# Kernel tuning notes

Hardware: AMD Instinct MI355X
Metric: run time of the kernel (lower is better)

## Reference

```python
import jax, jax.numpy as jnp
from jax import lax
import numpy as np

KSIZE = 3      # match-patch size
STRIDE = 1
RATE = 2       # down/up-sampling rate
FUSE_K = 3
SCALE = 10.0   # softmax scale
DN = ('NHWC', 'HWIO', 'NHWC')


def extract_patches(x, k, s):
    """tf.image.extract_patches(..., padding='SAME'); returns [B, L, k, k, C]."""
    B, H, W, C = x.shape
    oh, ow = -(-H // s), -(-W // s)
    ph = max((oh - 1) * s + k - H, 0)
    pw = max((ow - 1) * s + k - W, 0)
    xp = jnp.pad(x, ((0, 0), (ph // 2, ph - ph // 2), (pw // 2, pw - pw // 2), (0, 0)))
    cols = [xp[:, i:i + oh * s:s, j:j + ow * s:s, :] for i in range(k) for j in range(k)]
    p = jnp.stack(cols, axis=3)                 # [B, oh, ow, k*k, C]
    return p.reshape(B, oh * ow, k, k, C)


def setup_inputs() -> dict:
    key = jax.random.key(0)
    k1, k2, k3 = jax.random.split(key, 3)
    B, H, W, C = 4, 96, 96, 64
    f = jax.random.normal(k1, (B, H, W, C), jnp.float32)
    b = jax.random.normal(k2, (B, H, W, C), jnp.float32)
    mask = jnp.zeros((B, H, W, 1), jnp.float32)          # 0 = no hole -> all patches valid
    fuse_weight = jax.random.normal(k3, (FUSE_K, FUSE_K, 1, 1), jnp.float32) * 0.3
    return {"f": f, "b": b, "mask": mask, "fuse_weight": fuse_weight}


def reference(f, b, mask, fuse_weight):
    B, H, W, C = f.shape
    kernel = 2 * RATE
    # deconv kernels from full-res background: [B, 4, 4, C, L]
    raw_w = extract_patches(b, kernel, RATE * STRIDE).transpose(0, 2, 3, 4, 1)
    fd = f[:, 1::2, 1::2, :]
    bd = b[:, 1::2, 1::2, :]
    md = mask[:, 1::2, 1::2, :]
    h, w_ = fd.shape[1], fd.shape[2]
    L = h * w_
    # matching kernels from downscaled background: [B, 3, 3, C, L]
    wk = extract_patches(bd, KSIZE, STRIDE).transpose(0, 2, 3, 4, 1)
    # mask patches -> per-patch validity mm: [B, L]
    mp = extract_patches(md, KSIZE, STRIDE)
    mm = (jnp.mean(mp, axis=(2, 3, 4)) == 0.0).astype(f.dtype)

    def per_sample(xi, wi, rwi, mmi):
        # xi: [h, w, C]; wi: [3,3,C,L]; rwi: [4,4,C,L]; mmi: [L]
        norm = jnp.maximum(jnp.sqrt(jnp.sum(wi * wi, axis=(0, 1, 2))), 1e-4)
        yi = lax.conv_general_dilated(xi[None], wi / norm, (1, 1), 'SAME',
                                      dimension_numbers=DN)[0]        # [h, w, L]
        # fuse: 3x3 conv over flattened [HW, HW] score map, twice (transposed view)
        y = yi.reshape(1, L, L, 1)
        y = lax.conv_general_dilated(y, fuse_weight, (1, 1), 'SAME', dimension_numbers=DN)
        y = y.reshape(h, w_, h, w_).transpose(1, 0, 3, 2).reshape(1, L, L, 1)
        y = lax.conv_general_dilated(y, fuse_weight, (1, 1), 'SAME', dimension_numbers=DN)
        y = y.reshape(w_, h, w_, h).transpose(1, 0, 3, 2).reshape(h, w_, L)
        # mask-gated scaled softmax over background patches
        y = y * mmi
        y = jax.nn.softmax(y * SCALE, axis=-1) * mmi
        # deconv-style combine with raw 4x4 patches, stride=rate
        out = lax.conv_transpose(y[None], rwi, (RATE, RATE), 'SAME',
                                 dimension_numbers=DN, transpose_kernel=True)[0] / 4.0
        return out                                                    # [H, W, C]

    return jax.vmap(per_sample)(fd, wk, raw_w, mm)
```

## Files before the change

### kernel.cpp

```cpp
#include <hip/hip_runtime.h>
#include <hip/hip_bf16.h>

#define KL  2304
#define KC  64
#define KHS 48
#define KHH 96
#define OFFY (KHS*(KL + 1))

typedef __attribute__((ext_vector_type(8))) short bf16x8;
typedef __attribute__((ext_vector_type(4))) short bf16x4;
typedef __attribute__((ext_vector_type(8))) _Float16 f16x8;
typedef __attribute__((ext_vector_type(4))) _Float16 f16x4;
typedef __attribute__((ext_vector_type(4))) float f32x4;

static __device__ inline unsigned short f2bf(float x) {
    __hip_bfloat16 h = __float2bfloat16(x);
    return *reinterpret_cast<unsigned short*>(&h);
}
static __device__ inline float bf2f(unsigned short u) {
    unsigned v = ((unsigned)u) << 16;
    return __uint_as_float(v);
}
static __device__ inline unsigned short f2h(float x) {
    _Float16 h = (_Float16)x;
    return *reinterpret_cast<unsigned short*>(&h);
}
static __device__ inline float h2f(unsigned short u) {
    _Float16 h = *reinterpret_cast<_Float16*>(&u);
    return (float)h;
}

__global__ __launch_bounds__(64) void k_prep2(const float* __restrict__ f,
    const float* __restrict__ bsrc, const float* __restrict__ mask,
    float* __restrict__ nbuf, float* __restrict__ mdd,
    unsigned short* __restrict__ Ahat, unsigned short* __restrict__ Bhat)
{
    int blk = blockIdx.x;
    int p = blk % KL, bi = blk / KL;
    int y = p / KHS, x = p % KHS;
    int fy = 2*y + 1;
    int c = threadIdx.x;
    unsigned short* Ap = Ahat + ((size_t)bi*KL + p)*192;
    unsigned short* Bp = Bhat + ((size_t)bi*KL + p)*192;
    float bc = 0.f;
    #pragma unroll
    for (int dxi = 0; dxi < 3; dxi++) {
        int xx = x + dxi - 1;
        float av = 0.f, bv = 0.f;
        if ((unsigned)xx < KHS) {
            int fxx = 2*xx + 1;
            size_t src = (((size_t)bi*KHH + fy)*KHH + fxx)*KC + c;
            av = f[src]; bv = bsrc[src];
        }
        if (dxi == 1) bc = bv;
        Ap[dxi*64 + c] = f2h(av);
        Bp[dxi*64 + c] = f2h(bv);
    }
    float s = bc*bc;
    #pragma unroll
    for (int off = 32; off > 0; off >>= 1) s += __shfl_down(s, off);
    if (c == 0) {
        nbuf[bi*KL + p] = s;
        mdd[bi*KL + p]  = mask[((size_t)bi*KHH + fy)*KHH + (2*x + 1)];
    }
}

__global__ __launch_bounds__(256) void k_normmask(const float* __restrict__ nbuf,
    const float* __restrict__ mdd, float* __restrict__ rnrm, float* __restrict__ mm)
{
    int i = blockIdx.x*256 + threadIdx.x;
    int q = i % KL, bi = i / KL;
    int v = q / KHS, u = q % KHS;
    float sn = 0.f, sm = 0.f;
    for (int dy = -1; dy <= 1; dy++) {
        int vv = v + dy; if ((unsigned)vv >= KHS) continue;
        for (int dx = -1; dx <= 1; dx++) {
            int uu = u + dx; if ((unsigned)uu >= KHS) continue;
            sn += nbuf[bi*KL + vv*KHS + uu];
            sm += mdd[bi*KL + vv*KHS + uu];
        }
    }
    rnrm[i] = 1.0f / fmaxf(sqrtf(sn), 1e-4f);
    mm[i]   = (sm == 0.0f) ? 1.0f : 0.0f;
}

template<int KITERS, int OUTMODE, bool INFP16>
__global__ __launch_bounds__(256) void k_mfma_bt(const unsigned short* __restrict__ A,
    const unsigned short* __restrict__ B, void* __restrict__ Cv,
    int Ncols, size_t sA, size_t sB, size_t sC, int KDIM, int nsplit, size_t psize)
{
    int flat = blockIdx.x + gridDim.x*(blockIdx.y + gridDim.y*blockIdx.z);
    int nxy = gridDim.x*gridDim.y;
    int per = (nxy*gridDim.z) >> 3;
    int g = (flat & 7)*per + (flat >> 3);
    int z = g / nxy; int r = g - z*nxy;
    int by = r / gridDim.x; int bx = r - by*gridDim.x;

    int ks = z % nsplit, bi = z / nsplit;
    int kbase = ks * KITERS * 32;
    int n0 = bx*128, m0 = by*128;
    const unsigned short* Ab = A + (size_t)bi*sA;
    const unsigned short* Bb = B + (size_t)bi*sB;
    __shared__ unsigned short As[128*32];
    __shared__ unsigned short Bs[128*32];
    int t = threadIdx.x;
    int lane = t & 63, w = t >> 6;
    int l15 = lane & 15, quad = lane >> 4;
    int swf = (l15 >> 2) & 3;
    int wm = (w >> 1)*64, wn = (w & 1)*64;
    int srow = lane >> 2;
    int ch = lane & 3;
    f32x4 acc[4][4];
    #pragma unroll
    for (int i = 0; i < 4; i++)
        #pragma unroll
        for (int j = 0; j < 4; j++) acc[i][j] = (f32x4){0.f,0.f,0.f,0.f};

    for (int kk = 0; kk < KITERS; kk++) {
        int k0 = kbase + kk*32;
        #pragma unroll
        for (int i = 0; i < 2; i++) {
            int rbase = w*32 + i*16;
            int r2 = rbase + srow;
            int cs = (ch ^ ((r2 >> 2) & 3))*8;
            const unsigned short* ga = &Ab[(size_t)(m0 + r2)*KDIM + k0 + cs];
            __builtin_amdgcn_global_load_lds(
                (const __attribute__((address_space(1))) void*)ga,
                (__attribute__((address_space(3))) void*)&As[rbase*32], 16, 0, 0);
            const unsigned short* gb = &Bb[(size_t)(n0 + r2)*KDIM + k0 + cs];
            __builtin_amdgcn_global_load_lds(
                (const __attribute__((address_space(1))) void*)gb,
                (__attribute__((address_space(3))) void*)&Bs[rbase*32], 16, 0, 0);
        }
        __syncthreads();
        if (INFP16) {
            f16x8 af[4], bfr[4];
            #pragma unroll
            for (int mi = 0; mi < 4; mi++)
                af[mi] = *(const f16x8*)&As[(wm + mi*16 + l15)*32 + ((quad ^ swf)*8)];
            #pragma unroll
            for (int ni = 0; ni < 4; ni++)
                bfr[ni] = *(const f16x8*)&Bs[(wn + ni*16 + l15)*32 + ((quad ^ swf)*8)];
            #pragma unroll
            for (int mi = 0; mi < 4; mi++)
                #pragma unroll
                for (int ni = 0; ni < 4; ni++)
                    acc[mi][ni] = __builtin_amdgcn_mfma_f32_16x16x32_f16(
                        af[mi], bfr[ni], acc[mi][ni], 0, 0, 0);
        } else {
            bf16x8 af[4], bfr[4];
            #pragma unroll
            for (int mi = 0; mi < 4; mi++)
                af[mi] = *(const bf16x8*)&As[(wm + mi*16 + l15)*32 + ((quad ^ swf)*8)];
            #pragma unroll
            for (int ni = 0; ni < 4; ni++)
                bfr[ni] = *(const bf16x8*)&Bs[(wn + ni*16 + l15)*32 + ((quad ^ swf)*8)];
            #pragma unroll
            for (int mi = 0; mi < 4; mi++)
                #pragma unroll
                for (int ni = 0; ni < 4; ni++)
                    acc[mi][ni] = __builtin_amdgcn_mfma_f32_16x16x32_bf16(
                        af[mi], bfr[ni], acc[mi][ni], 0, 0, 0);
        }
        __syncthreads();
    }
    if (OUTMODE == 1 || OUTMODE == 2) {
        unsigned short* Cb = (unsigned short*)Cv + (size_t)ks*psize + (size_t)bi*sC;
        #pragma unroll
        for (int mi = 0; mi < 4; mi++)
            #pragma unroll
            for (int ni = 0; ni < 4; ni++) {
                int col = n0 + wn + ni*16 + l15;
                #pragma unroll
                for (int r2 = 0; r2 < 4; r2++) {
                    int row = m0 + wm + mi*16 + quad*4 + r2;
                    Cb[(size_t)row*Ncols + col] = (OUTMODE == 1)
                        ? f2bf(acc[mi][ni][r2]) : f2h(acc[mi][ni][r2]);
                }
            }
    } else {
        float* Cb = (float*)Cv + (size_t)ks*psize + (size_t)bi*sC;
        #pragma unroll
        for (int mi = 0; mi < 4; mi++)
            #pragma unroll
            for (int ni = 0; ni < 4; ni++) {
                int col = n0 + wn + ni*16 + l15;
                #pragma unroll
                for (int r2 = 0; r2 < 4; r2++) {
                    int row = m0 + wm + mi*16 + quad*4 + r2;
                    Cb[(size_t)row*Ncols + col] = acc[mi][ni][r2];
                }
            }
    }
}

#define KP_NT 18
#define STGA4(tt, j) do {                                                      \
    __builtin_amdgcn_global_load_lds(                                          \
        (const __attribute__((address_space(1))) void*)(gA + (size_t)(j)*128*2304 + (size_t)(tt)*32), \
        (__attribute__((address_space(3))) void*)&Atile[(tt)&3][((j)*128 + (w<<4))*32], 16, 0, 0); \
} while (0)
#define STGB4(tt, j) do {                                                      \
    __builtin_amdgcn_global_load_lds(                                          \
        (const __attribute__((address_space(1))) void*)(gB + (size_t)(j)*128*2304 + (size_t)(tt)*32), \
        (__attribute__((address_space(3))) void*)&Btile[(tt)&3][((j)*128 + (w<<4))*32], 16, 0, 0); \
} while (0)

#define MFMA_B(a, b, c) __builtin_amdgcn_mfma_f32_16x16x32_bf16(a, b, c, 0, 0, 0)

#define KT_BODY(kt, BVU, BVF) do {                                             \
    const unsigned short* At = &Atile[(kt) & 3][0];                            \
                                                          \
    __builtin_amdgcn_s_barrier();                                              \
    _Pragma("unroll")                                                          \
    for (int i = 0; i < 4; i++)                                                \
        af1[i] = *(const bf16x8*)&At[aOff + 2048 + i*512];                     \
    if ((kt) + 3 < KP_NT) { STGA4((kt)+3, 0); STGA4((kt)+3, 1); }              \
    __builtin_amdgcn_s_setprio(1);                                             \
    _Pragma("unroll")                                                          \
    for (int mi = 0; mi < 4; mi++)                                             \
        _Pragma("unroll")                                                      \
        for (int ni = 0; ni < 4; ni++)                                         \
            acc[mi][ni] = MFMA_B(af0[mi], BVU[ni], acc[mi][ni]);               \
    __builtin_amdgcn_s_setprio(0);                                             \
                                                          \
    __builtin_amdgcn_s_barrier();                                              \
    if ((kt) < KP_NT-1) {                                                      \
        if ((kt) <= KP_NT-4)      asm volatile("s_waitcnt vmcnt(6)" ::: "memory"); \
        else if ((kt) == KP_NT-3) asm volatile("s_waitcnt vmcnt(4)" ::: "memory"); \
        else                      asm volatile("s_waitcnt vmcnt(0)" ::: "memory"); \
        __builtin_amdgcn_sched_barrier(0);                                     \
        const unsigned short* An = &Atile[((kt)+1) & 3][0];                    \
        const unsigned short* Bn = &Btile[((kt)+1) & 3][0];                    \
        _Pragma("unroll")                                                      \
        for (int i = 0; i < 4; i++)                                            \
            af0[i] = *(const bf16x8*)&An[aOff + i*512];                        \
        _Pragma("unroll")                                                      \
        for (int ni = 0; ni < 4; ni++)                                         \
            BVF[ni] = *(const bf16x8*)&Bn[bOff + ni*512];                      \
    }                                                                          \
    if ((kt) + 3 < KP_NT) { STGB4((kt)+3, 0); STGB4((kt)+3, 1); }              \
    __builtin_amdgcn_s_setprio(1);                                             \
    _Pragma("unroll")                                                          \
    for (int mi = 0; mi < 4; mi++)                                             \
        _Pragma("unroll")                                                      \
        for (int ni = 0; ni < 4; ni++)                                         \
            acc[4+mi][ni] = MFMA_B(af1[mi], BVU[ni], acc[4+mi][ni]);           \
    __builtin_amdgcn_s_setprio(0);                                             \
} while (0)

__global__ __launch_bounds__(512, 2) void k_p8(
    const unsigned short* __restrict__ A,
    const unsigned short* __restrict__ B,
    unsigned short* __restrict__ C,
    size_t psize)
{
    __shared__ unsigned short Atile[4][8192];
    __shared__ unsigned short Btile[4][8192];

    int flat = blockIdx.x + gridDim.x*(blockIdx.y + gridDim.y*blockIdx.z);
    int nwg = gridDim.x*gridDim.y*gridDim.z;
    int cpx = nwg >> 3;
    int g = (flat & 7)*cpx + (flat >> 3);
    int nxy = gridDim.x*gridDim.y;
    int z = g / nxy; int rg = g - z*nxy;
    int by = rg / gridDim.x; int bx = rg - by*gridDim.x;

    int ks = z & 3, bi = z >> 2;
    int kbase = ks * 576;
    int m0 = by * 256, n0 = bx * 256;
    const unsigned short* Ab = A + (size_t)bi * (2304ull*2304);
    const unsigned short* Bb = B + (size_t)bi * (1024ull*2304);

    int t = threadIdx.x;
    int w = t >> 6, lane = t & 63;
    int wr = w >> 2, wc = w & 3;
    int l15 = lane & 15, quad = lane >> 4;

    int scol = ((t & 3) ^ ((t >> 3) & 3))*8;
    const unsigned short* gA = Ab + (size_t)(m0 + (t >> 2))*2304 + kbase + scol;
    const unsigned short* gB = Bb + (size_t)(n0 + (t >> 2))*2304 + kbase + scol;

    int csw = (quad ^ ((l15 >> 1) & 3))*8;
    int aOff = (wr*128 + l15)*32 + csw;
    int bOff = (wc*64  + l15)*32 + csw;

    f32x4 acc[8][4];
    #pragma unroll
    for (int mi = 0; mi < 8; mi++)
        #pragma unroll
        for (int ni = 0; ni < 4; ni++) acc[mi][ni] = (f32x4){0.f,0.f,0.f,0.f};

    #pragma unroll
    for (int tt = 0; tt < 3; tt++) {
        STGA4(tt, 0); STGA4(tt, 1);
        STGB4(tt, 0); STGB4(tt, 1);
    }
    asm volatile("s_waitcnt vmcnt(8)" ::: "memory");
    __builtin_amdgcn_s_barrier();

    bf16x8 af0[4], af1[4], bvA[4], bvB[4];
    #pragma unroll
    for (int i = 0; i < 4; i++)
        af0[i] = *(const bf16x8*)&Atile[0][aOff + i*512];
    #pragma unroll
    for (int ni = 0; ni < 4; ni++)
        bvA[ni] = *(const bf16x8*)&Btile[0][bOff + ni*512];

    #pragma unroll 1
    for (int ktp = 0; ktp < KP_NT/2; ktp++) {
        int kt0 = ktp*2;
        KT_BODY(kt0,     bvA, bvB);
        KT_BODY(kt0 + 1, bvB, bvA);
    }

    unsigned short* Cb = C + (size_t)ks*psize + (size_t)bi*(2304ull*1024);
    #pragma unroll
    for (int mi = 0; mi < 8; mi++)
        #pragma unroll
        for (int ni = 0; ni < 4; ni++) {
            int col = n0 + wc*64 + ni*16 + l15;
            int rowb = m0 + wr*128 + mi*16 + quad*4;
            #pragma unroll
            for (int r = 0; r < 4; r++)
                Cb[(size_t)(rowb + r)*1024 + col] = f2bf(acc[mi][ni][r]);
        }
}

__global__ __launch_bounds__(256) void k_fuse_a2(const unsigned short* __restrict__ T,
    const float* __restrict__ rnrm, const float* __restrict__ fw,
    unsigned short* __restrict__ Y1)
{
    __shared__ float Sl[10][280];
    int flat = blockIdx.x + 9*(blockIdx.y + 288*blockIdx.z);
    int nwg = 2592*gridDim.z;
    int cpx = nwg >> 3;
    int g = (flat & 7)*cpx + (flat >> 3);
    int bi = g / 2592; int rem = g - bi*2592;
    int by = rem / 9;  int qt = rem - by*9;

    int p0 = by*8, q0 = qt*256;
    const unsigned short* Tb = T + (size_t)bi*KL*KL;
    const float* rn = rnrm + bi*KL;
    int t = threadIdx.x;
    bool edge = (qt == 0) | (qt == 8);
    if (!edge) {
        for (int idx = t; idx < 10*34; idx += 256) {
            int r = idx / 34, j = idx - r*34;
            int pp = p0 - 1 + r;
            int qq0 = q0 - 8 + j*8;
            float s[8];
            #pragma unroll
            for (int k = 0; k < 8; k++) s[k] = 0.f;
            if ((unsigned)pp < KL) {
                size_t base = (size_t)pp*KL + qq0;
                bool bm = (pp >= KHS), bp = (pp < KL - KHS);
                size_t offm = bm ? (size_t)OFFY : 0;
                size_t offp = bp ? (size_t)OFFY : 0;
                float fm = bm ? 1.f : 0.f, fp2 = bp ? 1.f : 0.f;
                f16x8 v0 = *(const f16x8*)&Tb[base];
                f16x8 vm = *(const f16x8*)&Tb[base - offm];
                f16x8 vp = *(const f16x8*)&Tb[base + offp];
                #pragma unroll
                for (int k = 0; k < 8; k++)
                    s[k] = ((float)v0[k] + fm*(float)vm[k] + fp2*(float)vp[k]) * rn[qq0 + k];
            }
            #pragma unroll
            for (int k = 0; k < 8; k++) Sl[r][j*8 + k] = s[k];
        }
    } else {
        for (int idx = t; idx < 10*272; idx += 256) {
            int r = idx / 272, c = idx - r*272;
            int pp = p0 - 1 + r, qq = q0 - 8 + c;
            float s = 0.f;
            if ((unsigned)pp < KL && (unsigned)qq < KL) {
                size_t base = (size_t)pp*KL + qq;
                float acc = h2f(Tb[base]);
                if (pp >= KHS && qq >= KHS)         acc += h2f(Tb[base - OFFY]);
                if (pp < KL - KHS && qq < KL - KHS) acc += h2f(Tb[base + OFFY]);
                s = acc * rn[qq];
            }
            Sl[r][c] = s;
        }
    }
    __syncthreads();
    float w[9];
    #pragma unroll
    for (int i = 0; i < 9; i++) w[i] = fw[i];
    int q = q0 + t;
    float h0[10], h1[10], h2[10];
    #pragma unroll
    for (int r = 0; r < 10; r++) {
        float s0 = Sl[r][t+7], s1 = Sl[r][t+8], s2 = Sl[r][t+9];
        h0[r] = w[0]*s0 + w[1]*s1 + w[2]*s2;
        h1[r] = w[3]*s0 + w[4]*s1 + w[5]*s2;
        h2[r] = w[6]*s0 + w[7]*s1 + w[8]*s2;
    }
    #pragma unroll
    for (int rr = 0; rr < 8; rr++) {
        Y1[((size_t)bi*KL + p0 + rr)*KL + q] = f2h(h0[rr] + h1[rr+1] + h2[rr+2]);
    }
}

__global__ __launch_bounds__(256) void k_fuse_b(const unsigned short* __restrict__ Y1,
    const float* __restrict__ fw, const float* __restrict__ mm,
    unsigned short* __restrict__ Ybf)
{
    __shared__ float rowb[6][KL];
    int blk = blockIdx.x;
    int tp0 = (blk % 576)*4;
    int bi  = blk / 576;
    int t = threadIdx.x;
    const unsigned short* Yb = Y1 + (size_t)bi*KL*KL;
    for (int idx = t; idx < 6*(KL/8); idx += 256) {
        int a = idx / (KL/8), i = idx - a*(KL/8);
        int t2 = tp0 - 1 + a;
        if ((unsigned)t2 < KL) {
            int pr = (t2 % KHS)*KHS + t2/KHS;
            f16x8 v = *(const f16x8*)&Yb[(size_t)pr*KL + i*8];
            #pragma unroll
            for (int j = 0; j < 8; j++) rowb[a][i*8 + j] = (float)v[j];
        } else {
            #pragma unroll
            for (int j = 0; j < 8; j++) rowb[a][i*8 + j] = 0.f;
        }
    }
    float w9[9];
    #pragma unroll
    for (int i = 0; i < 9; i++) w9[i] = fw[i];
    __syncthreads();
    int w = t >> 6, lane = t & 63;
    int tp = tp0 + w;
    int x = tp / KHS, y = tp - x*KHS;
    int p = y*KHS + x;
    const float* mmb = mm + bi*KL;
    float vals[36];
    float lmax = -1e30f;
    #pragma unroll
    for (int i = 0; i < 36; i++) {
        int q = lane + i*64;
        int qm = (q >= KHS)      ? q - KHS : 2255 + q;
        int qp = (q <= KL-1-KHS) ? q + KHS : q - 2255;
        float fm = (q != 0)    ? 1.f : 0.f;
        float fp = (q != KL-1) ? 1.f : 0.f;
        float am = w9[0]*rowb[w][qm] + w9[3]*rowb[w+1][qm] + w9[6]*rowb[w+2][qm];
        float a0 = w9[1]*rowb[w][q]  + w9[4]*rowb[w+1][q]  + w9[7]*rowb[w+2][q];
        float ap = w9[2]*rowb[w][qp] + w9[5]*rowb[w+1][qp] + w9[8]*rowb[w+2][qp];
        float val = (fm*am + a0 + fp*ap) * mmb[q] * 10.0f;
        vals[i] = val;
        lmax = fmaxf(lmax, val);
    }
    #pragma unroll
    for (int off = 32; off > 0; off >>= 1) lmax = fmaxf(lmax, __shfl_down(lmax, off));
    lmax = __shfl(lmax, 0);
    float lsum = 0.f;
    #pragma unroll
    for (int i = 0; i < 36; i++) {
        float e = __expf(vals[i] - lmax);
        vals[i] = e;
        lsum += e;
    }
    #pragma unroll
    for (int off = 32; off > 0; off >>= 1) lsum += __shfl_down(lsum, off);
    lsum = __shfl(lsum, 0);
    float inv = 1.0f / lsum;
    unsigned short* orow = Ybf + ((size_t)bi*KL + p)*KL;
    #pragma unroll
    for (int i = 0; i < 36; i++) {
        int q = lane + i*64;
        orow[q] = f2bf(vals[i]*inv*mmb[q]);
    }
}

__global__ __launch_bounds__(256) void k_buildRt(const float* __restrict__ bsrc,
    unsigned short* __restrict__ Rt)
{
    int idx = blockIdx.x*256 + threadIdx.x;
    int k8 = idx % 288;
    int rest = idx / 288;
    int n  = rest % 1024;
    int bi = rest / 1024;
    int jj = n >> 6, c = n & 63;
    int ky = jj >> 2, kx = jj & 3;
    int k0 = k8*8;
    bf16x8 vv;
    #pragma unroll
    for (int j = 0; j < 8; j++) {
        int q = k0 + j;
        int v = q / KHS, u = q % KHS;
        int ry = 2*v + ky - 1, rx = 2*u + kx - 1;
        float val = 0.f;
        if ((unsigned)ry < KHH && (unsigned)rx < KHH)
            val = bsrc[(((size_t)bi*KHH + ry)*KHH + rx)*KC + c];
        vv[j] = (short)f2bf(val);
    }
    *(bf16x8*)&Rt[((size_t)bi*1024 + n)*KL + k0] = vv;
}

__global__ __launch_bounds__(256) void k_overlap(const unsigned short* __restrict__ P,
    float* __restrict__ out, size_t psize)
{
    size_t gid = (size_t)blockIdx.x*256 + threadIdx.x;
    int c4 = (int)(gid & 15)*4;
    size_t r = gid >> 4;
    int ix = (int)(r % KHH); r /= KHH;
    int iy = (int)(r % KHH);
    int bi = (int)(r / KHH);
    f32x4 acc = (f32x4){0.f,0.f,0.f,0.f};
    #pragma unroll
    for (int sy = 0; sy < 2; sy++) {
        int ky = (iy & 1) ? (sy*2) : (sy*2 + 1);
        int yp = (iy + 1 - ky) >> 1;
        if ((unsigned)yp >= KHS) continue;
        #pragma unroll
        for (int sx = 0; sx < 2; sx++) {
            int kx = (ix & 1) ? (sx*2) : (sx*2 + 1);
            int xp = (ix + 1 - kx) >> 1;
            if ((unsigned)xp >= KHS) continue;
            size_t idx = (((size_t)bi*KL + yp*KHS + xp)*16 + (ky*4 + kx))*64 + c4;
            #pragma unroll
            for (int s = 0; s < 4; s++) {
                bf16x4 v = *(const bf16x4*)&P[idx + s*psize];
                #pragma unroll
                for (int j = 0; j < 4; j++)
                    acc[j] += bf2f((unsigned short)v[j]);
            }
        }
    }
    f32x4 o = acc * 0.25f;
    *(f32x4*)&out[(((size_t)bi*KHH + iy)*KHH + ix)*KC + c4] = o;
}

extern "C" void kernel_launch(void* const* d_in, const int* in_sizes, int n_in,
                              void* d_out, int out_size, void* d_ws, size_t ws_size,
                              hipStream_t stream)
{
    const float* f    = (const float*)d_in[0];
    const float* b    = (const float*)d_in[1];
    const float* mask = (const float*)d_in[2];
    const float* fw   = (const float*)d_in[3];
    float* out = (float*)d_out;

    auto need = [](int nbc) -> size_t {
        return (size_t)nbc * (2ull*KL*KC + 4ull*KL + 2ull*(size_t)KL*KL) * 4ull;
    };
    int nbc = 4;
    if (need(nbc) > ws_size) nbc = 2;
    if (need(nbc) > ws_size) nbc = 1;

    for (int bi0 = 0; bi0 < 4; bi0 += nbc) {
        int nb = (4 - bi0 < nbc) ? (4 - bi0) : nbc;
        const float* fc = f    + (size_t)bi0*KHH*KHH*KC;
        const float* bc = b    + (size_t)bi0*KHH*KHH*KC;
        const float* mc = mask + (size_t)bi0*KHH*KHH;
        float* outc = out + (size_t)bi0*KHH*KHH*KC;

        float* w    = (float*)d_ws;
        float* nbuf = w;  w += (size_t)nbc*KL;
        float* mdd  = w;  w += (size_t)nbc*KL;
        float* rnrm = w;  w += (size_t)nbc*KL;
        float* mmb  = w;  w += (size_t)nbc*KL;
        float* bufA = w;  w += (size_t)nbc*KL*KL;
        float* bufB = w;
        unsigned short* Ahat = (unsigned short*)bufB;
        unsigned short* Bhat = Ahat + (size_t)nbc*KL*192;
        unsigned short* Tbuf = (unsigned short*)bufA;
        unsigned short* Y1   = (unsigned short*)bufB;
        unsigned short* Ybf = (unsigned short*)bufA;
        unsigned short* Rtb = Ybf + (size_t)nbc*KL*KL;
        unsigned short* Pbuf = (unsigned short*)bufB;
        size_t psize = (size_t)nbc*KL*1024;

        k_prep2     <<<nb*KL, 64, 0, stream>>>(fc, bc, mc, nbuf, mdd, Ahat, Bhat);
        k_normmask  <<<(nb*KL)/256, 256, 0, stream>>>(nbuf, mdd, rnrm, mmb);
        k_mfma_bt<6,2,true><<<dim3(18, 18, nb), 256, 0, stream>>>(
            Ahat, Bhat, Tbuf, KL, (size_t)KL*192, (size_t)KL*192, (size_t)KL*KL,
            192, 1, 0);
        k_fuse_a2   <<<dim3(9, 288, nb), 256, 0, stream>>>(Tbuf, rnrm, fw, Y1);
        k_fuse_b    <<<nb*576, 256, 0, stream>>>(Y1, fw, mmb, Ybf);
        k_buildRt   <<<(nb*1024*288)/256, 256, 0, stream>>>(bc, Rtb);
        k_p8<<<dim3(4, 9, nb*4), 512, 0, stream>>>(Ybf, Rtb, Pbuf, psize);
        k_overlap   <<<nb*KL/4*16/16, 256, 0, stream>>>(Pbuf, outc, psize);
    }
}
```

Before: 281.8 us.

## Load B operand straight to registers and cut split-K from four to three

The main GEMM stops staging B tiles through LDS. Each wave now loads its B fragments directly from global memory into registers two k-steps ahead, which removes one barrier per k-step and halves the LDS footprint. The split-K factor drops from 4 to 3 (24 k-tiles per slice), so the overlap kernel sums three partial buffers instead of four. The XCD remapping now handles workgroup counts not divisible by 8, and the prep kernel packs four pixels per 256-thread block. In exchange, the direct global loads of B are not shared across waves, which raises global traffic and register pressure.

```diff
diff --git a/kernel.cpp b/kernel.cpp
--- a/kernel.cpp
+++ b/kernel.cpp
@@ -30,16 +30,16 @@
     return (float)h;
 }
 
-__global__ __launch_bounds__(64) void k_prep2(const float* __restrict__ f,
+__global__ __launch_bounds__(256) void k_prep2(const float* __restrict__ f,
     const float* __restrict__ bsrc, const float* __restrict__ mask,
     float* __restrict__ nbuf, float* __restrict__ mdd,
     unsigned short* __restrict__ Ahat, unsigned short* __restrict__ Bhat)
 {
-    int blk = blockIdx.x;
-    int p = blk % KL, bi = blk / KL;
+    int pp = blockIdx.x*4 + (threadIdx.x >> 6);
+    int c = threadIdx.x & 63;
+    int p = pp % KL, bi = pp / KL;
     int y = p / KHS, x = p % KHS;
     int fy = 2*y + 1;
-    int c = threadIdx.x;
     unsigned short* Ap = Ahat + ((size_t)bi*KL + p)*192;
     unsigned short* Bp = Bhat + ((size_t)bi*KL + p)*192;
     float bc = 0.f;
@@ -194,28 +194,36 @@
     }
 }
 
-#define KP_NT 18
+#define KP_NT 24
 #define STGA4(tt, j) do {                                                      \
     __builtin_amdgcn_global_load_lds(                                          \
         (const __attribute__((address_space(1))) void*)(gA + (size_t)(j)*128*2304 + (size_t)(tt)*32), \
         (__attribute__((address_space(3))) void*)&Atile[(tt)&3][((j)*128 + (w<<4))*32], 16, 0, 0); \
 } while (0)
-#define STGB4(tt, j) do {                                                      \
-    __builtin_amdgcn_global_load_lds(                                          \
-        (const __attribute__((address_space(1))) void*)(gB + (size_t)(j)*128*2304 + (size_t)(tt)*32), \
-        (__attribute__((address_space(3))) void*)&Btile[(tt)&3][((j)*128 + (w<<4))*32], 16, 0, 0); \
+
+#define BLD(tt, BV) do {                                                       \
+    _Pragma("unroll")                                                          \
+    for (int ni = 0; ni < 4; ni++) {                                           \
+        const unsigned short* _a = gBn[ni] + (size_t)(tt)*32;                  \
+        asm volatile("global_load_dwordx4 %0, %1, off"                         \
+                     : "=v"(BV[ni]) : "v"(_a));                                \
+    }                                                                          \
 } while (0)
 
 #define MFMA_B(a, b, c) __builtin_amdgcn_mfma_f32_16x16x32_bf16(a, b, c, 0, 0, 0)
 
-#define KT_BODY(kt, BVU, BVF) do {                                             \
+#define KT_BODY(kt, BVU) do {                                                  \
     const unsigned short* At = &Atile[(kt) & 3][0];                            \
-                                                          \
     __builtin_amdgcn_s_barrier();                                              \
     _Pragma("unroll")                                                          \
     for (int i = 0; i < 4; i++)                                                \
         af1[i] = *(const bf16x8*)&At[aOff + 2048 + i*512];                     \
     if ((kt) + 3 < KP_NT) { STGA4((kt)+3, 0); STGA4((kt)+3, 1); }              \
+    if ((kt) <= KP_NT-4)      asm volatile("s_waitcnt vmcnt(8)" ::: "memory"); \
+    else if ((kt) == KP_NT-3) asm volatile("s_waitcnt vmcnt(6)" ::: "memory"); \
+    else if ((kt) == KP_NT-2) asm volatile("s_waitcnt vmcnt(4)" ::: "memory"); \
+    else                      asm volatile("s_waitcnt vmcnt(0)" ::: "memory"); \
+    __builtin_amdgcn_sched_barrier(0);                                         \
     __builtin_amdgcn_s_setprio(1);                                             \
     _Pragma("unroll")                                                          \
     for (int mi = 0; mi < 4; mi++)                                             \
@@ -223,23 +231,12 @@
         for (int ni = 0; ni < 4; ni++)                                         \
             acc[mi][ni] = MFMA_B(af0[mi], BVU[ni], acc[mi][ni]);               \
     __builtin_amdgcn_s_setprio(0);                                             \
-                                                          \
-    __builtin_amdgcn_s_barrier();                                              \
     if ((kt) < KP_NT-1) {                                                      \
-        if ((kt) <= KP_NT-4)      asm volatile("s_waitcnt vmcnt(6)" ::: "memory"); \
-        else if ((kt) == KP_NT-3) asm volatile("s_waitcnt vmcnt(4)" ::: "memory"); \
-        else                      asm volatile("s_waitcnt vmcnt(0)" ::: "memory"); \
-        __builtin_amdgcn_sched_barrier(0);                                     \
         const unsigned short* An = &Atile[((kt)+1) & 3][0];                    \
-        const unsigned short* Bn = &Btile[((kt)+1) & 3][0];                    \
         _Pragma("unroll")                                                      \
         for (int i = 0; i < 4; i++)                                            \
             af0[i] = *(const bf16x8*)&An[aOff + i*512];                        \
-        _Pragma("unroll")                                                      \
-        for (int ni = 0; ni < 4; ni++)                                         \
-            BVF[ni] = *(const bf16x8*)&Bn[bOff + ni*512];                      \
     }                                                                          \
-    if ((kt) + 3 < KP_NT) { STGB4((kt)+3, 0); STGB4((kt)+3, 1); }              \
     __builtin_amdgcn_s_setprio(1);                                             \
     _Pragma("unroll")                                                          \
     for (int mi = 0; mi < 4; mi++)                                             \
@@ -247,6 +244,7 @@
         for (int ni = 0; ni < 4; ni++)                                         \
             acc[4+mi][ni] = MFMA_B(af1[mi], BVU[ni], acc[4+mi][ni]);           \
     __builtin_amdgcn_s_setprio(0);                                             \
+    if ((kt) + 2 < KP_NT) { BLD((kt)+2, BVU); }                                \
 } while (0)
 
 __global__ __launch_bounds__(512, 2) void k_p8(
@@ -256,18 +254,18 @@
     size_t psize)
 {
     __shared__ unsigned short Atile[4][8192];
-    __shared__ unsigned short Btile[4][8192];
 
     int flat = blockIdx.x + gridDim.x*(blockIdx.y + gridDim.y*blockIdx.z);
     int nwg = gridDim.x*gridDim.y*gridDim.z;
-    int cpx = nwg >> 3;
-    int g = (flat & 7)*cpx + (flat >> 3);
+    int qq = nwg >> 3, rr8 = nwg & 7;
+    int xcd = flat & 7, sub = flat >> 3;
+    int g = (xcd < rr8 ? xcd*(qq+1) : rr8*(qq+1) + (xcd - rr8)*qq) + sub;
     int nxy = gridDim.x*gridDim.y;
     int z = g / nxy; int rg = g - z*nxy;
     int by = rg / gridDim.x; int bx = rg - by*gridDim.x;
 
-    int ks = z & 3, bi = z >> 2;
-    int kbase = ks * 576;
+    int ks = z % 3, bi = z / 3;
+    int kbase = ks * 768;
     int m0 = by * 256, n0 = bx * 256;
     const unsigned short* Ab = A + (size_t)bi * (2304ull*2304);
     const unsigned short* Bb = B + (size_t)bi * (1024ull*2304);
@@ -279,11 +277,14 @@
 
     int scol = ((t & 3) ^ ((t >> 3) & 3))*8;
     const unsigned short* gA = Ab + (size_t)(m0 + (t >> 2))*2304 + kbase + scol;
-    const unsigned short* gB = Bb + (size_t)(n0 + (t >> 2))*2304 + kbase + scol;
+
+    const unsigned short* gBn[4];
+    #pragma unroll
+    for (int ni = 0; ni < 4; ni++)
+        gBn[ni] = Bb + (size_t)(n0 + wc*64 + ni*16 + l15)*2304 + kbase + quad*8;
 
     int csw = (quad ^ ((l15 >> 1) & 3))*8;
     int aOff = (wr*128 + l15)*32 + csw;
-    int bOff = (wc*64  + l15)*32 + csw;
 
     f32x4 acc[8][4];
     #pragma unroll
@@ -291,27 +292,25 @@
         #pragma unroll
         for (int ni = 0; ni < 4; ni++) acc[mi][ni] = (f32x4){0.f,0.f,0.f,0.f};
 
-    #pragma unroll
-    for (int tt = 0; tt < 3; tt++) {
-        STGA4(tt, 0); STGA4(tt, 1);
-        STGB4(tt, 0); STGB4(tt, 1);
-    }
-    asm volatile("s_waitcnt vmcnt(8)" ::: "memory");
+    bf16x8 af0[4], af1[4], bvA[4], bvB[4];
+
+    STGA4(0, 0); STGA4(0, 1);
+    STGA4(1, 0); STGA4(1, 1);
+    STGA4(2, 0); STGA4(2, 1);
+    BLD(0, bvA);
+    BLD(1, bvB);
+    asm volatile("s_waitcnt vmcnt(4)" ::: "memory");
+    __builtin_amdgcn_sched_barrier(0);
     __builtin_amdgcn_s_barrier();
-
-    bf16x8 af0[4], af1[4], bvA[4], bvB[4];
     #pragma unroll
     for (int i = 0; i < 4; i++)
         af0[i] = *(const bf16x8*)&Atile[0][aOff + i*512];
-    #pragma unroll
-    for (int ni = 0; ni < 4; ni++)
-        bvA[ni] = *(const bf16x8*)&Btile[0][bOff + ni*512];
 
     #pragma unroll 1
     for (int ktp = 0; ktp < KP_NT/2; ktp++) {
         int kt0 = ktp*2;
-        KT_BODY(kt0,     bvA, bvB);
-        KT_BODY(kt0 + 1, bvB, bvA);
+        KT_BODY(kt0,     bvA);
+        KT_BODY(kt0 + 1, bvB);
     }
 
     unsigned short* Cb = C + (size_t)ks*psize + (size_t)bi*(2304ull*1024);
@@ -519,7 +518,7 @@
             if ((unsigned)xp >= KHS) continue;
             size_t idx = (((size_t)bi*KL + yp*KHS + xp)*16 + (ky*4 + kx))*64 + c4;
             #pragma unroll
-            for (int s = 0; s < 4; s++) {
+            for (int s = 0; s < 3; s++) {
                 bf16x4 v = *(const bf16x4*)&P[idx + s*psize];
                 #pragma unroll
                 for (int j = 0; j < 4; j++)
@@ -571,7 +570,7 @@
         unsigned short* Pbuf = (unsigned short*)bufB;
         size_t psize = (size_t)nbc*KL*1024;
 
-        k_prep2     <<<nb*KL, 64, 0, stream>>>(fc, bc, mc, nbuf, mdd, Ahat, Bhat);
+        k_prep2     <<<nb*KL/4, 256, 0, stream>>>(fc, bc, mc, nbuf, mdd, Ahat, Bhat);
         k_normmask  <<<(nb*KL)/256, 256, 0, stream>>>(nbuf, mdd, rnrm, mmb);
         k_mfma_bt<6,2,true><<<dim3(18, 18, nb), 256, 0, stream>>>(
             Ahat, Bhat, Tbuf, KL, (size_t)KL*192, (size_t)KL*192, (size_t)KL*KL,
@@ -579,7 +578,7 @@
         k_fuse_a2   <<<dim3(9, 288, nb), 256, 0, stream>>>(Tbuf, rnrm, fw, Y1);
         k_fuse_b    <<<nb*576, 256, 0, stream>>>(Y1, fw, mmb, Ybf);
         k_buildRt   <<<(nb*1024*288)/256, 256, 0, stream>>>(bc, Rtb);
-        k_p8<<<dim3(4, 9, nb*4), 512, 0, stream>>>(Ybf, Rtb, Pbuf, psize);
+        k_p8<<<dim3(4, 9, nb*3), 512, 0, stream>>>(Ybf, Rtb, Pbuf, psize);
         k_overlap   <<<nb*KL/4*16/16, 256, 0, stream>>>(Pbuf, outc, psize);
     }
 }
```

After: 288.2 us. +2.3%, slower.
